# Performance work log

Hardware: AMD Instinct MI355X
Metric: run time of the kernel (lower is better)

Reference implementation:

```python
import jax, jax.numpy as jnp
import numpy as np

N = 768
SINGLE_DIM = 384
PAIR_DIM = 128
D = 16      # proj_dim per head
H = 12      # n_heads
P = 4       # n_query_points
PV = 8      # n_point_values


def _random_rotations(key, n):
    a = jax.random.normal(key, (n, 3, 3), dtype=jnp.float32)
    q, r = jnp.linalg.qr(a)
    d = jnp.sign(jnp.diagonal(r, axis1=-2, axis2=-1))
    q = q * d[:, None, :]
    det = jnp.linalg.det(q)
    return q * jnp.where(det < 0, -1.0, 1.0)[:, None, None]


def setup_inputs() -> dict:
    key = jax.random.key(0)
    ks = jax.random.split(key, 12)
    s = 0.02
    return {
        "single_rep": jax.random.normal(ks[0], (N, SINGLE_DIM), dtype=jnp.float32),
        "pair_rep": jax.random.normal(ks[1], (N, N, PAIR_DIM), dtype=jnp.float32),
        "rotations": _random_rotations(ks[2], N),
        "translations": jax.random.normal(ks[3], (N, 3), dtype=jnp.float32),
        "Wqkv": s * jax.random.normal(ks[4], (SINGLE_DIM, 3 * H * D), dtype=jnp.float32),
        "Wb": s * jax.random.normal(ks[5], (PAIR_DIM, H), dtype=jnp.float32),
        "Wqk_pts": s * jax.random.normal(ks[6], (SINGLE_DIM, 2 * H * P * 3), dtype=jnp.float32),
        "Wv_pts": s * jax.random.normal(ks[7], (SINGLE_DIM, H * PV * 3), dtype=jnp.float32),
        "gamma": 0.1 * jax.random.normal(ks[8], (H,), dtype=jnp.float32),
        "Wout": s * jax.random.normal(ks[9], (H * (PAIR_DIM + D + PV * 3 + PV), SINGLE_DIM), dtype=jnp.float32),
        "bout": jnp.zeros((SINGLE_DIM,), dtype=jnp.float32),
    }


def _apply_frames(rot, trans, pts):
    # pts: [N, P, H, 3] -> R @ pt + t per residue (dim 0)
    return jnp.einsum('nba,npha->nphb', rot, pts) + trans[:, None, None, :]


def _apply_frames_inv(rot, trans, pts):
    # R^T (pt - t)
    return jnp.einsum('nab,npha->nphb', rot, pts - trans[:, None, None, :])


def reference(single_rep, pair_rep, rotations, translations,
              Wqkv, Wb, Wqk_pts, Wv_pts, gamma, Wout, bout):
    n = single_rep.shape[0]
    sqrt_inv_dim = 1.0 / np.sqrt(D).astype(np.float32)
    w_C = np.sqrt(2.0 / (9.0 * P)).astype(np.float32)
    w_L = np.sqrt(1.0 / 3.0).astype(np.float32)

    qkv = single_rep @ Wqkv                       # [N, 3*H*D]
    q, k, v = jnp.split(qkv, 3, axis=-1)
    q = q.reshape(n, D, H)
    k = k.reshape(n, D, H)
    v = v.reshape(n, D, H)

    b = pair_rep @ Wb                             # [N, N, H]

    qk_pts = single_rep @ Wqk_pts
    q_pts, k_pts = jnp.split(qk_pts, 2, axis=-1)
    q_pts = jnp.moveaxis(q_pts.reshape(n, P, 3, H), -1, -2)   # [N, P, H, 3]
    k_pts = jnp.moveaxis(k_pts.reshape(n, P, 3, H), -1, -2)
    v_pts = jnp.moveaxis((single_rep @ Wv_pts).reshape(n, PV, 3, H), -1, -2)  # [N, PV, H, 3]

    qg = _apply_frames(rotations, translations, q_pts)  # [N, P, H, 3]
    kg = _apply_frames(rotations, translations, k_pts)

    # sum_{p,t} ||qg_i - kg_j||^2 via expansion (avoids [N,N,P,H,3])
    q_sq = jnp.sum(qg * qg, axis=(1, 3))                # [N, H]
    k_sq = jnp.sum(kg * kg, axis=(1, 3))                # [N, H]
    cross = jnp.einsum('ipht,jpht->ijh', qg, kg)        # [N, N, H]
    dist_logits = q_sq[:, None, :] + k_sq[None, :, :] - 2.0 * cross

    dp_logits = sqrt_inv_dim * jnp.einsum('idh,jdh->ijh', q, k) + b
    scale = gamma * (w_C / 2.0)                          # [H]
    a = jax.nn.softmax(w_L * (dp_logits - scale * dist_logits), axis=1)  # [N, N, H]

    out_pair = jnp.einsum('ijh,ijz->izh', a, pair_rep)   # [N, pair_dim, H]
    out_value = jnp.einsum('ijh,jdh->idh', a, v)          # [N, D, H]

    vg = _apply_frames(rotations, translations, v_pts)    # [N, PV, H, 3]
    op = jnp.einsum('ijh,jpht->ipht', a, vg)              # [N, PV, H, 3]
    out_points = _apply_frames_inv(rotations, translations, op)
    out_points_norm = jnp.linalg.norm(out_points, axis=-1)  # [N, PV, H]

    out = jnp.concatenate([
        out_pair.reshape(n, -1),
        out_value.reshape(n, -1),
        out_points.reshape(n, -1),
        out_points_norm.reshape(n, -1),
    ], axis=1)
    return out @ Wout + bout
```

## Files before the change

kernel.cpp:

```cpp
#include <hip/hip_runtime.h>
#include <math.h>

#define NN 768
#define SD 384
#define HH 12

#define W_L 0.57735026918962576f
#define W_C 0.23570226039551584f

typedef __attribute__((ext_vector_type(8))) short short8;
typedef __attribute__((ext_vector_type(4))) float floatx4;
typedef unsigned short ushort_t;
typedef unsigned int uint_t;

__device__ __forceinline__ float wave_max(float v){ for(int o=32;o;o>>=1) v=fmaxf(v,__shfl_xor(v,o)); return v; }
__device__ __forceinline__ float wave_sum(float v){ for(int o=32;o;o>>=1) v+=__shfl_xor(v,o); return v; }

static __device__ __forceinline__ ushort_t f2bf(float f) {
  union { float f; uint_t u; } v; v.f = f;
  uint_t r = (v.u + 0x7FFFu + ((v.u >> 16) & 1u)) >> 16;
  return (ushort_t)r;
}
static __device__ __forceinline__ uint_t pack2bf(float lo, float hi) {
  return ((uint_t)f2bf(hi) << 16) | (uint_t)f2bf(lo);
}

__global__ __launch_bounds__(256) void k1a_gemm(
    const float* __restrict__ single, const float* __restrict__ Wqkv,
    const float* __restrict__ Wqk, const float* __restrict__ Wvp,
    float* __restrict__ raw)
{
  __shared__ float Al[64][17];
  __shared__ float Bl[16][68];
  const int tid = threadIdx.x;
  const int bm = blockIdx.x / 18, bn = blockIdx.x % 18;
  const int tr = tid >> 4, tc = tid & 15;

  const int bcol = bn*64 + (tid & 15)*4;
  const float* Wsrc; int wstride;
  if (bcol < 576)      { Wsrc = Wqkv + bcol;        wstride = 576; }
  else if (bcol < 864) { Wsrc = Wqk  + (bcol-576);  wstride = 288; }
  else                 { Wsrc = Wvp  + (bcol-864);  wstride = 288; }
  const int brow = tid >> 4;
  const int ar = tid >> 2, ac = (tid & 3)*4;

  float4 acc0 = {0,0,0,0}, acc1 = {0,0,0,0}, acc2 = {0,0,0,0}, acc3 = {0,0,0,0};

  for (int kc = 0; kc < 24; ++kc) {
    __syncthreads();
    *(float4*)&Al[ar][ac] = *(const float4*)(single + (size_t)(bm*64+ar)*SD + kc*16 + ac);
    *(float4*)&Bl[brow][(tid&15)*4] = *(const float4*)(Wsrc + (size_t)(kc*16+brow)*wstride);
    __syncthreads();
    #pragma unroll
    for (int kk = 0; kk < 16; ++kk) {
      float a0 = Al[tr*4+0][kk], a1 = Al[tr*4+1][kk], a2 = Al[tr*4+2][kk], a3 = Al[tr*4+3][kk];
      float4 bv = *(float4*)&Bl[kk][tc*4];
      acc0.x += a0*bv.x; acc0.y += a0*bv.y; acc0.z += a0*bv.z; acc0.w += a0*bv.w;
      acc1.x += a1*bv.x; acc1.y += a1*bv.y; acc1.z += a1*bv.z; acc1.w += a1*bv.w;
      acc2.x += a2*bv.x; acc2.y += a2*bv.y; acc2.z += a2*bv.z; acc2.w += a2*bv.w;
      acc3.x += a3*bv.x; acc3.y += a3*bv.y; acc3.z += a3*bv.z; acc3.w += a3*bv.w;
    }
  }
  float* o = raw + (size_t)(bm*64 + tr*4)*1152 + bn*64 + tc*4;
  *(float4*)(o)            = acc0;
  *(float4*)(o + 1152)     = acc1;
  *(float4*)(o + 2*1152)   = acc2;
  *(float4*)(o + 3*1152)   = acc3;
}

__global__ __launch_bounds__(256) void k1b_pack(
    const float* __restrict__ raw_g, const float* __restrict__ rot,
    const float* __restrict__ trans, const float* __restrict__ gamma,
    float* __restrict__ Qt, ushort_t* __restrict__ Ktb, ushort_t* __restrict__ vvT)
{
  __shared__ float raw[4][1152];
  __shared__ float gbuf[4][16][HH][3];
  const int tid = threadIdx.x;
  const int i0 = blockIdx.x * 4;

  for (int s = tid; s < 4*288; s += 256) {
    int r = s / 288, q = s % 288;
    *(float4*)(&raw[r][q*4]) = *(const float4*)(raw_g + (size_t)(i0+r)*1152 + q*4);
  }
  __syncthreads();

  for (int s = tid; s < 4*576; s += 256) {
    int r = s / 576, cc = s % 576;
    int d = (cc % 192) / HH, h = cc % HH;
    int i = i0 + r;
    float val = raw[r][cc];
    if (cc < 192)       Qt[(size_t)i*384 + h*32 + d] = 0.25f*W_L*val;
    else if (cc < 384)  Ktb[(size_t)i*384 + h*32 + d] = f2bf(val);
    else                vvT[(size_t)(h*40 + d)*768 + i] = f2bf(val);
  }
  for (int s = tid; s < 768; s += 256) {
    int r = s / 192, rem = s % 192;
    int slot = rem / HH, h = rem % HH;
    int i = i0 + r;
    int base;
    if (slot < 4) base = 576 + slot*36;
    else if (slot < 8) base = 720 + (slot-4)*36;
    else base = 864 + (slot-8)*36;
    float x0 = raw[r][base + 0*12 + h];
    float x1 = raw[r][base + 1*12 + h];
    float x2 = raw[r][base + 2*12 + h];
    const float* R = rot + (size_t)i*9;
    const float* T = trans + (size_t)i*3;
    float g0 = R[0]*x0 + R[1]*x1 + R[2]*x2 + T[0];
    float g1 = R[3]*x0 + R[4]*x1 + R[5]*x2 + T[1];
    float g2 = R[6]*x0 + R[7]*x1 + R[8]*x2 + T[2];
    gbuf[r][slot][h][0]=g0; gbuf[r][slot][h][1]=g1; gbuf[r][slot][h][2]=g2;
    if (slot < 4) {
      float sc2 = 2.0f*W_L*(gamma[h]*W_C*0.5f);
      float* q = Qt + (size_t)i*384 + h*32 + 16 + slot*3;
      q[0]=sc2*g0; q[1]=sc2*g1; q[2]=sc2*g2;
    } else if (slot < 8) {
      ushort_t* k = Ktb + (size_t)i*384 + h*32 + 16 + (slot-4)*3;
      k[0]=f2bf(g0); k[1]=f2bf(g1); k[2]=f2bf(g2);
    } else {
      ushort_t* vp = vvT + (size_t)(h*40 + 16 + (slot-8)*3)*768 + i;
      vp[0]=f2bf(g0); vp[768]=f2bf(g1); vp[2*768]=f2bf(g2);
    }
  }
  __syncthreads();
  for (int s = tid; s < 96; s += 256) {
    int r = s / 24, rem = s % 24;
    int h = rem / 2, qk = rem % 2;
    int i = i0 + r;
    float sum = 0;
    int b0 = qk ? 4 : 0;
    for (int p = 0; p < 4; ++p)
      for (int t = 0; t < 3; ++t) { float g = gbuf[r][b0+p][h][t]; sum += g*g; }
    float sc = gamma[h]*W_C*0.5f;
    if (qk == 0) {
      float* q = Qt + (size_t)i*384 + h*32;
      q[28] = -W_L*sc; q[29] = -W_L*sc*sum; q[30] = 0.f; q[31] = 0.f;
    } else {
      ushort_t* k = Ktb + (size_t)i*384 + h*32;
      k[28] = f2bf(sum); k[29] = f2bf(1.f); k[30] = 0; k[31] = 0;
    }
  }
}

#define TJS 140
__global__ __launch_bounds__(256, 3) void k2t_logits(
    const float* __restrict__ pair, const float* __restrict__ Wb,
    const float* __restrict__ Qt, const ushort_t* __restrict__ Ktb,
    float* __restrict__ L, ushort_t* __restrict__ Tzg)
{
  __shared__ ushort_t Tj[64*TJS];
  __shared__ ushort_t WbT[16*136];
  __shared__ float Qrow[384];
  const int tid = threadIdx.x;
  const int i = blockIdx.x / 12;
  const int j0 = (blockIdx.x % 12) * 64;
  const int lane = tid & 63;
  const int w = tid >> 6;
  const int co = lane & 15, gg = lane >> 4;
  const int jb = w*16;

  for (int s = tid; s < 1536; s += 256) {
    int z = s / 12, h = s % 12;
    WbT[h*136 + z] = f2bf(W_L * Wb[s]);
  }
  for (int s = tid; s < 544; s += 256) WbT[1632 + s] = 0;
  for (int s = tid; s < 384; s += 256) Qrow[s] = Qt[(size_t)i*384 + s];

  short8 kf[12];
  {
    const ushort_t* kr = Ktb + (size_t)(j0 + jb + co)*384;
    #pragma unroll
    for (int kt = 0; kt < 12; ++kt)
      kf[kt] = *(const short8*)(kr + kt*32 + gg*8);
  }

  const float* src = pair + ((size_t)i*NN + j0)*128;
  float4 pv[8];
  #pragma unroll
  for (int k = 0; k < 8; ++k) {
    int f = tid + k*256;
    int row = f >> 5, zq = f & 31;
    pv[k] = *(const float4*)(src + (size_t)row*128 + zq*4);
  }
  #pragma unroll
  for (int k = 0; k < 8; ++k) {
    int f = tid + k*256;
    int row = f >> 5, zq = f & 31;
    uint_t* d = (uint_t*)&Tj[row*TJS + zq*4];
    d[0] = pack2bf(pv[k].x, pv[k].y);
    d[1] = pack2bf(pv[k].z, pv[k].w);
  }
  __syncthreads();

  short8 z8, myQ, wb[4];
  #pragma unroll
  for (int s = 0; s < 8; ++s) z8[s] = 0;
  #pragma unroll
  for (int s = 0; s < 8; ++s)
    myQ[s] = (co < 12) ? (short)f2bf(Qrow[co*32 + gg*8 + s]) : (short)0;
  #pragma unroll
  for (int kt = 0; kt < 4; ++kt)
    wb[kt] = *(const short8*)&WbT[co*136 + kt*32 + gg*8];

  floatx4 D; D[0]=0.f; D[1]=0.f; D[2]=0.f; D[3]=0.f;
  #pragma unroll
  for (int kt = 0; kt < 4; ++kt) {
    short8 a = *(const short8*)&Tj[(jb+co)*TJS + kt*32 + gg*8];
    D = __builtin_amdgcn_mfma_f32_16x16x32_bf16(a, wb[kt], D, 0, 0, 0);
  }
  #pragma unroll
  for (int kt = 0; kt < 12; ++kt) {
    short8 b = (co == kt) ? myQ : z8;
    D = __builtin_amdgcn_mfma_f32_16x16x32_bf16(kf[kt], b, D, 0, 0, 0);
  }
  if (co < 12) {
    float4 st = {D[0], D[1], D[2], D[3]};
    *(float4*)(L + ((size_t)i*12 + co)*768 + j0 + jb + gg*4) = st;
  }

  const int z = tid & 127, jg = tid >> 7;
  uint_t ow[16];
  #pragma unroll
  for (int m = 0; m < 16; ++m) {
    ushort_t a = Tj[(jg*32 + 2*m)*TJS + z];
    ushort_t b = Tj[(jg*32 + 2*m + 1)*TJS + z];
    ow[m] = ((uint_t)b << 16) | (uint_t)a;
  }
  ushort_t* dst = Tzg + ((size_t)i*128 + z)*768 + j0 + jg*32;
  #pragma unroll
  for (int q = 0; q < 4; ++q) {
    uint4 u4 = {ow[q*4+0], ow[q*4+1], ow[q*4+2], ow[q*4+3]};
    *(uint4*)(dst + q*8) = u4;
  }
}

#define PTS 544
__global__ __launch_bounds__(512, 4) void k3g(
    const float* __restrict__ L, const ushort_t* __restrict__ Tzg,
    const ushort_t* __restrict__ vvT, const float* __restrict__ rot,
    const float* __restrict__ trans, float* __restrict__ C2)
{
  __shared__ ushort_t PTb[24*PTS];
  __shared__ float oacc[480];
  const int tid = threadIdx.x;
  const int i = (NN - 1) - blockIdx.x;
  const int w = tid >> 6, lane = tid & 63;
  const int co = lane & 15, gg = lane >> 4;

  const float* Lr = L + (size_t)i*12*768;
  #pragma unroll
  for (int m = 0; m < 2; ++m) {
    if (m == 1 && w >= 4) break;
    const int h = (m == 0) ? w : 8 + w;
    const float* row = Lr + (size_t)h*768;
    float mx = -1e30f;
    #pragma unroll
    for (int k = 0; k < 12; ++k) mx = fmaxf(mx, row[lane + 64*k]);
    mx = wave_max(mx);
    float ev[12]; float sm = 0.f;
    #pragma unroll
    for (int k = 0; k < 12; ++k) { ev[k] = __expf(row[lane + 64*k] - mx); sm += ev[k]; }
    sm = wave_sum(sm);
    const float inv = 1.0f / sm;
    #pragma unroll
    for (int k = 0; k < 12; ++k) {
      int jj = lane + 64*k;
      PTb[(jj >> 5)*PTS + h*34 + (jj & 31)] = f2bf(ev[k]*inv);
    }
  }
  for (int s = tid; s < 24*136; s += 512) {
    int t = s / 136, r = s % 136;
    PTb[t*PTS + 408 + r] = 0;
  }
  __syncthreads();

  floatx4 accZ; accZ[0]=0.f; accZ[1]=0.f; accZ[2]=0.f; accZ[3]=0.f;
  floatx4 accV[4];
  #pragma unroll
  for (int u = 0; u < 4; ++u) { accV[u][0]=0.f; accV[u][1]=0.f; accV[u][2]=0.f; accV[u][3]=0.f; }

  const bool full = (w*4 + 2 < 30);
  const ushort_t* tz  = Tzg + ((size_t)i*128 + w*16 + co)*768 + gg*8;
  const ushort_t* vb0 = vvT + (size_t)((w*4+0)*16 + co)*768 + gg*8;
  const ushort_t* vb1 = vvT + (size_t)((w*4+1)*16 + co)*768 + gg*8;
  const ushort_t* vb2 = vvT + (size_t)((w*4+2)*16 + co)*768 + gg*8;
  const ushort_t* vb3 = vvT + (size_t)((w*4+3)*16 + co)*768 + gg*8;

  short8 aT  = *(const short8*)(tz);
  short8 aV0 = *(const short8*)(vb0);
  short8 aV1 = *(const short8*)(vb1);
  short8 aV2 = aT, aV3 = aT;
  short8 bT  = *(const short8*)(tz  + 32);
  short8 bV0 = *(const short8*)(vb0 + 32);
  short8 bV1 = *(const short8*)(vb1 + 32);
  short8 bV2 = bT, bV3 = bT;
  if (full) {
    aV2 = *(const short8*)(vb2);      aV3 = *(const short8*)(vb3);
    bV2 = *(const short8*)(vb2 + 32); bV3 = *(const short8*)(vb3 + 32);
  }

  #pragma unroll 1
  for (int tt = 0; tt < 24; tt += 2) {
    {
      const short8 aP = *(const short8*)&PTb[tt*PTS + co*34 + gg*8];
      accZ    = __builtin_amdgcn_mfma_f32_16x16x32_bf16(aP, aT,  accZ,    0, 0, 0);
      accV[0] = __builtin_amdgcn_mfma_f32_16x16x32_bf16(aP, aV0, accV[0], 0, 0, 0);
      accV[1] = __builtin_amdgcn_mfma_f32_16x16x32_bf16(aP, aV1, accV[1], 0, 0, 0);
      if (full) {
        accV[2] = __builtin_amdgcn_mfma_f32_16x16x32_bf16(aP, aV2, accV[2], 0, 0, 0);
        accV[3] = __builtin_amdgcn_mfma_f32_16x16x32_bf16(aP, aV3, accV[3], 0, 0, 0);
      }
    }
    if (tt + 2 < 24) {
      const int toff = (tt+2)*32;
      aT  = *(const short8*)(tz  + toff);
      aV0 = *(const short8*)(vb0 + toff);
      aV1 = *(const short8*)(vb1 + toff);
      if (full) {
        aV2 = *(const short8*)(vb2 + toff);
        aV3 = *(const short8*)(vb3 + toff);
      }
    }
    {
      const short8 aP = *(const short8*)&PTb[(tt+1)*PTS + co*34 + gg*8];
      accZ    = __builtin_amdgcn_mfma_f32_16x16x32_bf16(aP, bT,  accZ,    0, 0, 0);
      accV[0] = __builtin_amdgcn_mfma_f32_16x16x32_bf16(aP, bV0, accV[0], 0, 0, 0);
      accV[1] = __builtin_amdgcn_mfma_f32_16x16x32_bf16(aP, bV1, accV[1], 0, 0, 0);
      if (full) {
        accV[2] = __builtin_amdgcn_mfma_f32_16x16x32_bf16(aP, bV2, accV[2], 0, 0, 0);
        accV[3] = __builtin_amdgcn_mfma_f32_16x16x32_bf16(aP, bV3, accV[3], 0, 0, 0);
      }
    }
    if (tt + 3 < 24) {
      const int toff = (tt+3)*32;
      bT  = *(const short8*)(tz  + toff);
      bV0 = *(const short8*)(vb0 + toff);
      bV1 = *(const short8*)(vb1 + toff);
      if (full) {
        bV2 = *(const short8*)(vb2 + toff);
        bV3 = *(const short8*)(vb3 + toff);
      }
    }
  }

  float* o = C2 + (size_t)i*2112;
  #pragma unroll
  for (int r = 0; r < 4; ++r) {
    int h = gg*4 + r;
    if (h < 12) o[(w*16 + co)*12 + h] = accZ[r];
  }
  #pragma unroll
  for (int u = 0; u < 4; ++u) {
    int cb = w*4 + u;
    if (cb < 30) {
      int c = cb*16 + co;
      int hc = c / 40;
      #pragma unroll
      for (int r = 0; r < 4; ++r)
        if (gg*4 + r == hc) oacc[c] = accV[u][r];
    }
  }
  __syncthreads();

  if (tid < 96) {
    const int pp = tid / 12, hh = tid % 12;
    const float* R = rot + (size_t)i*9;
    const float* T = trans + (size_t)i*3;
    float x0 = oacc[hh*40+16+pp*3+0] - T[0];
    float x1 = oacc[hh*40+16+pp*3+1] - T[1];
    float x2 = oacc[hh*40+16+pp*3+2] - T[2];
    float y0 = R[0]*x0 + R[3]*x1 + R[6]*x2;
    float y1 = R[1]*x0 + R[4]*x1 + R[7]*x2;
    float y2 = R[2]*x0 + R[5]*x1 + R[8]*x2;
    o[1728 + pp*36 + hh*3 + 0] = y0;
    o[1728 + pp*36 + hh*3 + 1] = y1;
    o[1728 + pp*36 + hh*3 + 2] = y2;
    o[2016 + pp*12 + hh] = sqrtf(y0*y0 + y1*y1 + y2*y2);
  } else if (tid < 288) {
    const int c = tid - 96;
    int d = c / 12, hh = c % 12;
    o[1536 + d*12 + hh] = oacc[hh*40 + d];
  }
}

__global__ __launch_bounds__(256) void k5_out(
    const float* __restrict__ C2, const float* __restrict__ Wout,
    const float* __restrict__ bout, float* __restrict__ out)
{
  __shared__ float Al[32*68];
  __shared__ float Bl[64*36];
  const int tid = threadIdx.x;
  const int bm = blockIdx.x / 12, bn = blockIdx.x % 12;
  const int tr = tid / 16, tc = tid % 16;
  float acc00=0, acc01=0, acc10=0, acc11=0;
  for (int kc = 0; kc < 33; ++kc) {
    __syncthreads();
    for (int s = tid; s < 512; s += 256) {
      int row = s / 16, kq = s % 16;
      *(float4*)(&Al[row*68 + kq*4]) =
        *(const float4*)(C2 + (size_t)(bm*32+row)*2112 + kc*64 + kq*4);
    }
    for (int s = tid; s < 512; s += 256) {
      int kk = s / 8, cq = s % 8;
      *(float4*)(&Bl[kk*36 + cq*4]) =
        *(const float4*)(Wout + (size_t)(kc*64+kk)*384 + bn*32 + cq*4);
    }
    __syncthreads();
    for (int kk = 0; kk < 64; ++kk) {
      float a0 = Al[(tr*2)*68 + kk], a1 = Al[(tr*2+1)*68 + kk];
      float b0 = Bl[kk*36 + tc*2], b1 = Bl[kk*36 + tc*2 + 1];
      acc00 += a0*b0; acc01 += a0*b1;
      acc10 += a1*b0; acc11 += a1*b1;
    }
  }
  int r0 = bm*32 + tr*2, c0 = bn*32 + tc*2;
  out[(size_t)r0*384 + c0]       = acc00 + bout[c0];
  out[(size_t)r0*384 + c0+1]     = acc01 + bout[c0+1];
  out[(size_t)(r0+1)*384 + c0]   = acc10 + bout[c0];
  out[(size_t)(r0+1)*384 + c0+1] = acc11 + bout[c0+1];
}

extern "C" void kernel_launch(void* const* d_in, const int* in_sizes, int n_in,
                              void* d_out, int out_size, void* d_ws, size_t ws_size,
                              hipStream_t stream)
{
  const float* single = (const float*)d_in[0];
  const float* pair   = (const float*)d_in[1];
  const float* rot    = (const float*)d_in[2];
  const float* trans  = (const float*)d_in[3];
  const float* Wqkv   = (const float*)d_in[4];
  const float* Wb     = (const float*)d_in[5];
  const float* Wqk    = (const float*)d_in[6];
  const float* Wvp    = (const float*)d_in[7];
  const float* gamma  = (const float*)d_in[8];
  const float* Wout   = (const float*)d_in[9];
  const float* bout   = (const float*)d_in[10];

  float* ws   = (float*)d_ws;
  float* raw  = ws;
  float* Qt   = raw + (size_t)768*1152;
  float* C2   = Qt  + (size_t)768*384;
  float* L    = C2  + (size_t)768*2112;
  ushort_t* Ktb = (ushort_t*)(L + (size_t)768*12*768);
  ushort_t* vvT = Ktb + (size_t)768*384;
  ushort_t* Tzg = vvT + (size_t)480*768;
  float* out  = (float*)d_out;

  k1a_gemm<<<dim3(216), dim3(256), 0, stream>>>(single, Wqkv, Wqk, Wvp, raw);
  k1b_pack<<<dim3(192), dim3(256), 0, stream>>>(raw, rot, trans, gamma, Qt, Ktb, vvT);
  k2t_logits<<<dim3(9216), dim3(256), 0, stream>>>(pair, Wb, Qt, Ktb, L, Tzg);
  k3g<<<dim3(768), dim3(512), 0, stream>>>(L, Tzg, vvT, rot, trans, C2);
  k5_out<<<dim3(288), dim3(256), 0, stream>>>(C2, Wout, bout, out);
}
```

Before: 354.0 us.

## Split attention-apply kernel along j into four partial blocks with separate reduce

The single per-row attention kernel becomes three kernels. The first computes softmax max and inverse sum per row and head. The second launches four blocks per row, each covering a quarter of the j range and writing partial pair/value accumulators. The third sums the partials and applies the inverse frame transform. This raises the block count for better occupancy and latency hiding, at the cost of two extra launches, recomputing exp, and extra global traffic for the partials.

```diff
diff --git a/kernel.cpp b/kernel.cpp
--- a/kernel.cpp
+++ b/kernel.cpp
@@ -234,41 +234,61 @@
   }
 }
 
-#define PTS 544
-__global__ __launch_bounds__(512, 4) void k3g(
-    const float* __restrict__ L, const ushort_t* __restrict__ Tzg,
-    const ushort_t* __restrict__ vvT, const float* __restrict__ rot,
-    const float* __restrict__ trans, float* __restrict__ C2)
-{
-  __shared__ ushort_t PTb[24*PTS];
-  __shared__ float oacc[480];
-  const int tid = threadIdx.x;
-  const int i = (NN - 1) - blockIdx.x;
+__global__ __launch_bounds__(256) void k3s_stats(
+    const float* __restrict__ L, float* __restrict__ Sm, float* __restrict__ Si)
+{
+  const int i = blockIdx.x;
+  const int tid = threadIdx.x;
   const int w = tid >> 6, lane = tid & 63;
-  const int co = lane & 15, gg = lane >> 4;
-
   const float* Lr = L + (size_t)i*12*768;
   #pragma unroll
-  for (int m = 0; m < 2; ++m) {
-    if (m == 1 && w >= 4) break;
-    const int h = (m == 0) ? w : 8 + w;
+  for (int m = 0; m < 3; ++m) {
+    const int h = w + 4*m;
     const float* row = Lr + (size_t)h*768;
     float mx = -1e30f;
     #pragma unroll
     for (int k = 0; k < 12; ++k) mx = fmaxf(mx, row[lane + 64*k]);
     mx = wave_max(mx);
-    float ev[12]; float sm = 0.f;
+    float sm = 0.f;
     #pragma unroll
-    for (int k = 0; k < 12; ++k) { ev[k] = __expf(row[lane + 64*k] - mx); sm += ev[k]; }
+    for (int k = 0; k < 12; ++k) sm += __expf(row[lane + 64*k] - mx);
     sm = wave_sum(sm);
-    const float inv = 1.0f / sm;
+    if (lane == 0) { Sm[i*12 + h] = mx; Si[i*12 + h] = 1.0f/sm; }
+  }
+}
+
+#define PTS 544
+__global__ __launch_bounds__(512) void k3p_partial(
+    const float* __restrict__ L, const float* __restrict__ Sm,
+    const float* __restrict__ Si, const ushort_t* __restrict__ Tzg,
+    const ushort_t* __restrict__ vvT, float* __restrict__ PzZ,
+    float* __restrict__ PzV)
+{
+  __shared__ ushort_t PTb[6*PTS];
+  __shared__ float oacc[480];
+  const int tid = threadIdx.x;
+  const int bid = blockIdx.x;
+  const int i = (NN - 1) - (bid >> 2);
+  const int q = bid & 3;
+  const int w = tid >> 6, lane = tid & 63;
+  const int co = lane & 15, gg = lane >> 4;
+
+  const float* Lr = L + (size_t)i*12*768 + q*192;
+  #pragma unroll
+  for (int m = 0; m < 2; ++m) {
+    if (m == 1 && w >= 4) break;
+    const int h = (m == 0) ? w : 8 + w;
+    const float mh  = Sm[i*12 + h];
+    const float inv = Si[i*12 + h];
+    const float* row = Lr + (size_t)h*768;
     #pragma unroll
-    for (int k = 0; k < 12; ++k) {
+    for (int k = 0; k < 3; ++k) {
       int jj = lane + 64*k;
-      PTb[(jj >> 5)*PTS + h*34 + (jj & 31)] = f2bf(ev[k]*inv);
-    }
-  }
-  for (int s = tid; s < 24*136; s += 512) {
+      float p = __expf(row[jj] - mh) * inv;
+      PTb[(jj >> 5)*PTS + h*34 + (jj & 31)] = f2bf(p);
+    }
+  }
+  for (int s = tid; s < 6*136; s += 512) {
     int t = s / 136, r = s % 136;
     PTb[t*PTS + 408 + r] = 0;
   }
@@ -280,11 +300,11 @@
   for (int u = 0; u < 4; ++u) { accV[u][0]=0.f; accV[u][1]=0.f; accV[u][2]=0.f; accV[u][3]=0.f; }
 
   const bool full = (w*4 + 2 < 30);
-  const ushort_t* tz  = Tzg + ((size_t)i*128 + w*16 + co)*768 + gg*8;
-  const ushort_t* vb0 = vvT + (size_t)((w*4+0)*16 + co)*768 + gg*8;
-  const ushort_t* vb1 = vvT + (size_t)((w*4+1)*16 + co)*768 + gg*8;
-  const ushort_t* vb2 = vvT + (size_t)((w*4+2)*16 + co)*768 + gg*8;
-  const ushort_t* vb3 = vvT + (size_t)((w*4+3)*16 + co)*768 + gg*8;
+  const ushort_t* tz  = Tzg + ((size_t)i*128 + w*16 + co)*768 + q*192 + gg*8;
+  const ushort_t* vb0 = vvT + (size_t)((w*4+0)*16 + co)*768 + q*192 + gg*8;
+  const ushort_t* vb1 = vvT + (size_t)((w*4+1)*16 + co)*768 + q*192 + gg*8;
+  const ushort_t* vb2 = vvT + (size_t)((w*4+2)*16 + co)*768 + q*192 + gg*8;
+  const ushort_t* vb3 = vvT + (size_t)((w*4+3)*16 + co)*768 + q*192 + gg*8;
 
   short8 aT  = *(const short8*)(tz);
   short8 aV0 = *(const short8*)(vb0);
@@ -300,7 +320,7 @@
   }
 
   #pragma unroll 1
-  for (int tt = 0; tt < 24; tt += 2) {
+  for (int tt = 0; tt < 6; tt += 2) {
     {
       const short8 aP = *(const short8*)&PTb[tt*PTS + co*34 + gg*8];
       accZ    = __builtin_amdgcn_mfma_f32_16x16x32_bf16(aP, aT,  accZ,    0, 0, 0);
@@ -311,7 +331,7 @@
         accV[3] = __builtin_amdgcn_mfma_f32_16x16x32_bf16(aP, aV3, accV[3], 0, 0, 0);
       }
     }
-    if (tt + 2 < 24) {
+    if (tt + 2 < 6) {
       const int toff = (tt+2)*32;
       aT  = *(const short8*)(tz  + toff);
       aV0 = *(const short8*)(vb0 + toff);
@@ -331,7 +351,7 @@
         accV[3] = __builtin_amdgcn_mfma_f32_16x16x32_bf16(aP, bV3, accV[3], 0, 0, 0);
       }
     }
-    if (tt + 3 < 24) {
+    if (tt + 3 < 6) {
       const int toff = (tt+3)*32;
       bT  = *(const short8*)(tz  + toff);
       bV0 = *(const short8*)(vb0 + toff);
@@ -343,11 +363,11 @@
     }
   }
 
-  float* o = C2 + (size_t)i*2112;
+  const size_t pidx = (size_t)(i*4 + q);
   #pragma unroll
   for (int r = 0; r < 4; ++r) {
     int h = gg*4 + r;
-    if (h < 12) o[(w*16 + co)*12 + h] = accZ[r];
+    if (h < 12) PzZ[(pidx*12 + h)*128 + w*16 + co] = accZ[r];
   }
   #pragma unroll
   for (int u = 0; u < 4; ++u) {
@@ -359,6 +379,29 @@
       for (int r = 0; r < 4; ++r)
         if (gg*4 + r == hc) oacc[c] = accV[u][r];
     }
+  }
+  __syncthreads();
+  if (tid < 480) PzV[pidx*480 + tid] = oacc[tid];
+}
+
+__global__ __launch_bounds__(256) void k3r_reduce(
+    const float* __restrict__ PzZ, const float* __restrict__ PzV,
+    const float* __restrict__ rot, const float* __restrict__ trans,
+    float* __restrict__ C2)
+{
+  __shared__ float oacc[480];
+  const int i = blockIdx.x;
+  const int tid = threadIdx.x;
+  float* o = C2 + (size_t)i*2112;
+
+  for (int s = tid; s < 1536; s += 256) {
+    int h = s >> 7, z = s & 127;
+    const float* pz = PzZ + ((size_t)(i*4)*12 + h)*128 + z;
+    o[z*12 + h] = (pz[0] + pz[1536]) + (pz[2*1536] + pz[3*1536]);
+  }
+  for (int s = tid; s < 480; s += 256) {
+    const float* pv = PzV + (size_t)i*4*480 + s;
+    oacc[s] = (pv[0] + pv[480]) + (pv[960] + pv[1440]);
   }
   __syncthreads();
 
@@ -441,7 +484,11 @@
   float* Qt   = raw + (size_t)768*1152;
   float* C2   = Qt  + (size_t)768*384;
   float* L    = C2  + (size_t)768*2112;
-  ushort_t* Ktb = (ushort_t*)(L + (size_t)768*12*768);
+  float* Sm   = L   + (size_t)768*12*768;
+  float* Si   = Sm  + 9216;
+  float* PzZ  = Si  + 9216;
+  float* PzV  = PzZ + (size_t)768*4*12*128;
+  ushort_t* Ktb = (ushort_t*)(PzV + (size_t)768*4*480);
   ushort_t* vvT = Ktb + (size_t)768*384;
   ushort_t* Tzg = vvT + (size_t)480*768;
   float* out  = (float*)d_out;
@@ -449,6 +496,8 @@
   k1a_gemm<<<dim3(216), dim3(256), 0, stream>>>(single, Wqkv, Wqk, Wvp, raw);
   k1b_pack<<<dim3(192), dim3(256), 0, stream>>>(raw, rot, trans, gamma, Qt, Ktb, vvT);
   k2t_logits<<<dim3(9216), dim3(256), 0, stream>>>(pair, Wb, Qt, Ktb, L, Tzg);
-  k3g<<<dim3(768), dim3(512), 0, stream>>>(L, Tzg, vvT, rot, trans, C2);
+  k3s_stats<<<dim3(768), dim3(256), 0, stream>>>(L, Sm, Si);
+  k3p_partial<<<dim3(3072), dim3(512), 0, stream>>>(L, Sm, Si, Tzg, vvT, PzZ, PzV);
+  k3r_reduce<<<dim3(768), dim3(256), 0, stream>>>(PzZ, PzV, rot, trans, C2);
   k5_out<<<dim3(288), dim3(256), 0, stream>>>(C2, Wout, bout, out);
 }
```

Result: slower. 365.4 us (+3.2%).
